# Performance work log

Measured on AMD Instinct MI355X. Metric: run time of the kernel, lower is better.

Reference implementation:

```python
import jax, jax.numpy as jnp
import numpy as np

B, C, H, W = 4, 19, 1024, 1024
N = 500000

def setup_inputs() -> dict:
    key = jax.random.key(0)
    k1, k2, k3, k4, k5 = jax.random.split(key, 5)
    predict = jax.random.normal(k1, (B, C, H, W), dtype=jnp.float32)
    target = jax.random.randint(k2, (B, H, W), 0, C, dtype=jnp.int32)
    loc_b = jax.random.randint(k3, (N,), 0, B, dtype=jnp.int64)
    loc_row = jax.random.randint(k4, (N,), 0, H, dtype=jnp.int64)
    loc_col = jax.random.randint(k5, (N,), 0, W, dtype=jnp.int64)
    return {"predict": predict, "target": target,
            "loc_b": loc_b, "loc_row": loc_row, "loc_col": loc_col}

def reference(predict, target, loc_b, loc_row, loc_col):
    # Faithful to PartialLoss: full softmax over channel dim of the WHOLE
    # tensor, then gather sparse locations, then CrossEntropyLoss (which
    # internally applies log_softmax again to the probabilities).
    pred = jax.nn.softmax(predict, axis=1)            # [B, C, H, W]
    gathered = pred[loc_b, :, loc_row, loc_col]       # [N, C]
    labels = target[loc_b, loc_row, loc_col].astype(jnp.int32)  # [N]
    logp = jax.nn.log_softmax(gathered, axis=-1)      # [N, C]
    nll = -jnp.take_along_axis(logp, labels[:, None], axis=-1)[:, 0]  # [N]
    return jnp.mean(nll)
```

## Files before the change

kernel.cpp:

```cpp
#include <hip/hip_runtime.h>


#define CCH 19
#define BLOCK 256
#define POS_BITS 20
#define TOTAL_POS (4 << POS_BITS)

__device__ __forceinline__ float nll_from_channels(const float* __restrict__ base,
                                                   int label, size_t ch_stride)
{
    float x[CCH];
    #pragma unroll
    for (int j = 0; j < CCH; ++j) x[j] = base[(size_t)j * ch_stride];

    float m = x[0];
    #pragma unroll
    for (int j = 1; j < CCH; ++j) m = fmaxf(m, x[j]);

    float s = 0.0f, e_label = 0.0f;
    #pragma unroll
    for (int j = 0; j < CCH; ++j) {
        float e = __expf(x[j] - m);
        s += e;
        if (j == label) e_label = e;
        x[j] = e;
    }
    float inv = 1.0f / s;

    float s2 = 0.0f;
    #pragma unroll
    for (int j = 0; j < CCH; ++j) s2 += __expf(x[j] * inv);

    return __logf(s2) - e_label * inv;
}

__global__ __launch_bounds__(BLOCK) void nll_table_kernel(
    const float* __restrict__ predict,
    const int* __restrict__ target,
    float* __restrict__ table)
{
    int i = blockIdx.x * blockDim.x + threadIdx.x;
    if (i >= TOTAL_POS) return;
    int b = i >> POS_BITS;
    int pos = i & ((1 << POS_BITS) - 1);
    const float* base = predict + (((size_t)b * CCH) << POS_BITS) + (size_t)pos;
    table[i] = nll_from_channels(base, target[i], (size_t)1 << POS_BITS);
}

__global__ __launch_bounds__(BLOCK) void table_gather_kernel(
    const float* __restrict__ table,
    const int* __restrict__ loc_b,
    const int* __restrict__ loc_row,
    const int* __restrict__ loc_col,
    float* __restrict__ partial,
    int n)
{
    int i = blockIdx.x * blockDim.x + threadIdx.x;
    float nll = 0.0f;
    if (i < n) {
        int idx = (loc_b[i] << POS_BITS) + (loc_row[i] << 10) + loc_col[i];
        nll = table[idx];
    }
    __shared__ float red[BLOCK];
    red[threadIdx.x] = nll;
    __syncthreads();
    #pragma unroll
    for (int off = BLOCK / 2; off > 0; off >>= 1) {
        if (threadIdx.x < off) red[threadIdx.x] += red[threadIdx.x + off];
        __syncthreads();
    }
    if (threadIdx.x == 0) partial[blockIdx.x] = red[0];
}

__global__ __launch_bounds__(BLOCK) void partial_loss_gather(
    const float* __restrict__ predict,
    const int* __restrict__ target,
    const int* __restrict__ loc_b,
    const int* __restrict__ loc_row,
    const int* __restrict__ loc_col,
    float* __restrict__ partial,
    int n)
{
    int i = blockIdx.x * blockDim.x + threadIdx.x;
    float nll = 0.0f;
    if (i < n) {
        int b = loc_b[i];
        int pos = (loc_row[i] << 10) + loc_col[i];
        const float* base = predict + (((size_t)b * CCH) << POS_BITS) + (size_t)pos;
        int label = target[((size_t)b << POS_BITS) + (size_t)pos];
        nll = nll_from_channels(base, label, (size_t)1 << POS_BITS);
    }
    __shared__ float red[BLOCK];
    red[threadIdx.x] = nll;
    __syncthreads();
    #pragma unroll
    for (int off = BLOCK / 2; off > 0; off >>= 1) {
        if (threadIdx.x < off) red[threadIdx.x] += red[threadIdx.x + off];
        __syncthreads();
    }
    if (threadIdx.x == 0) partial[blockIdx.x] = red[0];
}

__global__ __launch_bounds__(BLOCK) void partial_loss_finalize(
    const float* __restrict__ partial,
    int nparts,
    float* __restrict__ out,
    float inv_n)
{
    __shared__ double red[BLOCK];
    double acc = 0.0;
    for (int i = threadIdx.x; i < nparts; i += BLOCK) acc += (double)partial[i];
    red[threadIdx.x] = acc;
    __syncthreads();
    #pragma unroll
    for (int off = BLOCK / 2; off > 0; off >>= 1) {
        if (threadIdx.x < off) red[threadIdx.x] += red[threadIdx.x + off];
        __syncthreads();
    }
    if (threadIdx.x == 0) out[0] = (float)(red[0] * (double)inv_n);
}

extern "C" void kernel_launch(void* const* d_in, const int* in_sizes, int n_in,
                              void* d_out, int out_size, void* d_ws, size_t ws_size,
                              hipStream_t stream)
{
    const float* predict = (const float*)d_in[0];
    const int*   target  = (const int*)d_in[1];
    const int*   loc_b   = (const int*)d_in[2];
    const int*   loc_row = (const int*)d_in[3];
    const int*   loc_col = (const int*)d_in[4];
    float* out = (float*)d_out;

    int n = in_sizes[2];
    int nblocks = (n + BLOCK - 1) / BLOCK;

    size_t table_bytes = (size_t)TOTAL_POS * sizeof(float);
    size_t partial_bytes = (size_t)nblocks * sizeof(float);

    if (ws_size >= table_bytes + partial_bytes) {
        float* table   = (float*)d_ws;
        float* partial = (float*)((char*)d_ws + table_bytes);
        int tblocks = (TOTAL_POS + BLOCK - 1) / BLOCK;
        nll_table_kernel<<<tblocks, BLOCK, 0, stream>>>(predict, target, table);
        table_gather_kernel<<<nblocks, BLOCK, 0, stream>>>(
            table, loc_b, loc_row, loc_col, partial, n);
        partial_loss_finalize<<<1, BLOCK, 0, stream>>>(
            partial, nblocks, out, 1.0f / (float)n);
    } else {
        float* partial = (float*)d_ws;
        partial_loss_gather<<<nblocks, BLOCK, 0, stream>>>(
            predict, target, loc_b, loc_row, loc_col, partial, n);
        partial_loss_finalize<<<1, BLOCK, 0, stream>>>(
            partial, nblocks, out, 1.0f / (float)n);
    }
}
```

Baseline: 87.75 us.

## Compute NLL table only for 16-position chunks touched by sampled locations

Adds a byte mask over 16-position chunks. It is cleared and built from the sampled locations, and the table kernel skips threads whose chunk is unmarked. This is meant to cut predict-tensor reads for positions never gathered. With 500k random samples over about 4M positions, most chunks are still touched, and memory lines may be shared with touched chunks, so the saving in traffic may be small. Two extra kernel launches and a scattered byte-write pass are added in exchange.

```diff
diff --git a/kernel.cpp b/kernel.cpp
--- a/kernel.cpp
+++ b/kernel.cpp
@@ -5,14 +5,10 @@
 #define BLOCK 256
 #define POS_BITS 20
 #define TOTAL_POS (4 << POS_BITS)
+#define NCHUNK (TOTAL_POS >> 4)
 
-__device__ __forceinline__ float nll_from_channels(const float* __restrict__ base,
-                                                   int label, size_t ch_stride)
+__device__ __forceinline__ float nll_compute(float* __restrict__ x, int label)
 {
-    float x[CCH];
-    #pragma unroll
-    for (int j = 0; j < CCH; ++j) x[j] = base[(size_t)j * ch_stride];
-
     float m = x[0];
     #pragma unroll
     for (int j = 1; j < CCH; ++j) m = fmaxf(m, x[j]);
@@ -34,17 +30,43 @@
     return __logf(s2) - e_label * inv;
 }
 
-__global__ __launch_bounds__(BLOCK) void nll_table_kernel(
+__global__ __launch_bounds__(BLOCK) void clear_mask(unsigned int* __restrict__ mask32)
+{
+    int i = blockIdx.x * blockDim.x + threadIdx.x;
+    mask32[i] = 0u;
+}
+
+__global__ __launch_bounds__(BLOCK) void build_mask(
+    const int* __restrict__ loc_b,
+    const int* __restrict__ loc_row,
+    const int* __restrict__ loc_col,
+    unsigned char* __restrict__ mask,
+    int n)
+{
+    int i = blockIdx.x * blockDim.x + threadIdx.x;
+    if (i < n) {
+        int idx = (loc_b[i] << POS_BITS) + (loc_row[i] << 10) + loc_col[i];
+        mask[idx >> 4] = 1;
+    }
+}
+
+__global__ __launch_bounds__(BLOCK) void nll_table_masked(
     const float* __restrict__ predict,
     const int* __restrict__ target,
+    const unsigned char* __restrict__ mask,
     float* __restrict__ table)
 {
     int i = blockIdx.x * blockDim.x + threadIdx.x;
-    if (i >= TOTAL_POS) return;
+    if (!mask[i >> 4]) return;
     int b = i >> POS_BITS;
     int pos = i & ((1 << POS_BITS) - 1);
     const float* base = predict + (((size_t)b * CCH) << POS_BITS) + (size_t)pos;
-    table[i] = nll_from_channels(base, target[i], (size_t)1 << POS_BITS);
+
+    float x[CCH];
+    #pragma unroll
+    for (int j = 0; j < CCH; ++j) x[j] = base[(size_t)j << POS_BITS];
+
+    table[i] = nll_compute(x, target[i]);
 }
 
 __global__ __launch_bounds__(BLOCK) void table_gather_kernel(
@@ -88,7 +110,10 @@
         int pos = (loc_row[i] << 10) + loc_col[i];
         const float* base = predict + (((size_t)b * CCH) << POS_BITS) + (size_t)pos;
         int label = target[((size_t)b << POS_BITS) + (size_t)pos];
-        nll = nll_from_channels(base, label, (size_t)1 << POS_BITS);
+        float x[CCH];
+        #pragma unroll
+        for (int j = 0; j < CCH; ++j) x[j] = base[(size_t)j << POS_BITS];
+        nll = nll_compute(x, label);
     }
     __shared__ float red[BLOCK];
     red[threadIdx.x] = nll;
@@ -134,14 +159,19 @@
     int n = in_sizes[2];
     int nblocks = (n + BLOCK - 1) / BLOCK;
 
-    size_t table_bytes = (size_t)TOTAL_POS * sizeof(float);
-    size_t partial_bytes = (size_t)nblocks * sizeof(float);
+    size_t table_bytes   = (size_t)TOTAL_POS * sizeof(float);
+    size_t partial_bytes = (size_t)((nblocks + 63) & ~63) * sizeof(float);
+    size_t mask_bytes    = (size_t)NCHUNK;
 
-    if (ws_size >= table_bytes + partial_bytes) {
-        float* table   = (float*)d_ws;
-        float* partial = (float*)((char*)d_ws + table_bytes);
-        int tblocks = (TOTAL_POS + BLOCK - 1) / BLOCK;
-        nll_table_kernel<<<tblocks, BLOCK, 0, stream>>>(predict, target, table);
+    if (ws_size >= table_bytes + partial_bytes + mask_bytes) {
+        float*         table   = (float*)d_ws;
+        float*         partial = (float*)((char*)d_ws + table_bytes);
+        unsigned char* mask    = (unsigned char*)d_ws + table_bytes + partial_bytes;
+
+        clear_mask<<<NCHUNK / 4 / BLOCK, BLOCK, 0, stream>>>((unsigned int*)mask);
+        build_mask<<<nblocks, BLOCK, 0, stream>>>(loc_b, loc_row, loc_col, mask, n);
+        nll_table_masked<<<TOTAL_POS / BLOCK, BLOCK, 0, stream>>>(
+            predict, target, mask, table);
         table_gather_kernel<<<nblocks, BLOCK, 0, stream>>>(
             table, loc_b, loc_row, loc_col, partial, n);
         partial_loss_finalize<<<1, BLOCK, 0, stream>>>(
```

New measurement: 95.34 us. 8.6% more time.

## Replace dense NLL table with per-position hit counts and masked reduction

Applied to the files above, without the earlier changes.

Instead of computing NLL for every pixel into a float table and then gathering it, the code builds a byte-packed histogram of how often each position is sampled, using atomics on 32-bit words. It then scans all positions, loads the 19 channels only where the count is nonzero, and accumulates count-weighted NLL directly into block partials. About 11% of positions are hit, so most channel loads are skipped. The trade-offs are an extra clear kernel, atomic contention, and 8-bit counters that would overflow past 255 hits per position.

```diff
diff --git a/kernel.cpp b/kernel.cpp
--- a/kernel.cpp
+++ b/kernel.cpp
@@ -5,14 +5,10 @@
 #define BLOCK 256
 #define POS_BITS 20
 #define TOTAL_POS (4 << POS_BITS)
+#define NBLK_A (TOTAL_POS / BLOCK)
 
-__device__ __forceinline__ float nll_from_channels(const float* __restrict__ base,
-                                                   int label, size_t ch_stride)
+__device__ __forceinline__ float nll_compute(float* __restrict__ x, int label)
 {
-    float x[CCH];
-    #pragma unroll
-    for (int j = 0; j < CCH; ++j) x[j] = base[(size_t)j * ch_stride];
-
     float m = x[0];
     #pragma unroll
     for (int j = 1; j < CCH; ++j) m = fmaxf(m, x[j]);
@@ -34,35 +30,47 @@
     return __logf(s2) - e_label * inv;
 }
 
-__global__ __launch_bounds__(BLOCK) void nll_table_kernel(
-    const float* __restrict__ predict,
-    const int* __restrict__ target,
-    float* __restrict__ table)
+__global__ __launch_bounds__(BLOCK) void clear_counts(unsigned int* __restrict__ cnt32)
 {
     int i = blockIdx.x * blockDim.x + threadIdx.x;
-    if (i >= TOTAL_POS) return;
-    int b = i >> POS_BITS;
-    int pos = i & ((1 << POS_BITS) - 1);
-    const float* base = predict + (((size_t)b * CCH) << POS_BITS) + (size_t)pos;
-    table[i] = nll_from_channels(base, target[i], (size_t)1 << POS_BITS);
+    cnt32[i] = 0u;
 }
 
-__global__ __launch_bounds__(BLOCK) void table_gather_kernel(
-    const float* __restrict__ table,
+__global__ __launch_bounds__(BLOCK) void build_counts(
     const int* __restrict__ loc_b,
     const int* __restrict__ loc_row,
     const int* __restrict__ loc_col,
-    float* __restrict__ partial,
+    unsigned int* __restrict__ cnt32,
     int n)
 {
     int i = blockIdx.x * blockDim.x + threadIdx.x;
-    float nll = 0.0f;
     if (i < n) {
         int idx = (loc_b[i] << POS_BITS) + (loc_row[i] << 10) + loc_col[i];
-        nll = table[idx];
+        atomicAdd(&cnt32[idx >> 2], 1u << ((idx & 3) << 3));
     }
+}
+
+__global__ __launch_bounds__(BLOCK) void nll_count_reduce(
+    const float* __restrict__ predict,
+    const int* __restrict__ target,
+    const unsigned char* __restrict__ counts,
+    float* __restrict__ partial)
+{
+    int i = blockIdx.x * blockDim.x + threadIdx.x;
+    int cnt = counts[i];
+    float contrib = 0.0f;
+    if (cnt) {
+        int b = i >> POS_BITS;
+        int pos = i & ((1 << POS_BITS) - 1);
+        const float* base = predict + (((size_t)b * CCH) << POS_BITS) + (size_t)pos;
+        float x[CCH];
+        #pragma unroll
+        for (int j = 0; j < CCH; ++j) x[j] = base[(size_t)j << POS_BITS];
+        contrib = (float)cnt * nll_compute(x, target[i]);
+    }
+
     __shared__ float red[BLOCK];
-    red[threadIdx.x] = nll;
+    red[threadIdx.x] = contrib;
     __syncthreads();
     #pragma unroll
     for (int off = BLOCK / 2; off > 0; off >>= 1) {
@@ -88,7 +96,10 @@
         int pos = (loc_row[i] << 10) + loc_col[i];
         const float* base = predict + (((size_t)b * CCH) << POS_BITS) + (size_t)pos;
         int label = target[((size_t)b << POS_BITS) + (size_t)pos];
-        nll = nll_from_channels(base, label, (size_t)1 << POS_BITS);
+        float x[CCH];
+        #pragma unroll
+        for (int j = 0; j < CCH; ++j) x[j] = base[(size_t)j << POS_BITS];
+        nll = nll_compute(x, label);
     }
     __shared__ float red[BLOCK];
     red[threadIdx.x] = nll;
@@ -134,18 +145,19 @@
     int n = in_sizes[2];
     int nblocks = (n + BLOCK - 1) / BLOCK;
 
-    size_t table_bytes = (size_t)TOTAL_POS * sizeof(float);
-    size_t partial_bytes = (size_t)nblocks * sizeof(float);
+    size_t count_bytes   = (size_t)TOTAL_POS;
+    size_t partial_bytes = (size_t)NBLK_A * sizeof(float);
 
-    if (ws_size >= table_bytes + partial_bytes) {
-        float* table   = (float*)d_ws;
-        float* partial = (float*)((char*)d_ws + table_bytes);
-        int tblocks = (TOTAL_POS + BLOCK - 1) / BLOCK;
-        nll_table_kernel<<<tblocks, BLOCK, 0, stream>>>(predict, target, table);
-        table_gather_kernel<<<nblocks, BLOCK, 0, stream>>>(
-            table, loc_b, loc_row, loc_col, partial, n);
+    if (ws_size >= count_bytes + partial_bytes) {
+        unsigned int* cnt32   = (unsigned int*)d_ws;
+        float*        partial = (float*)((char*)d_ws + count_bytes);
+
+        clear_counts<<<TOTAL_POS / 4 / BLOCK, BLOCK, 0, stream>>>(cnt32);
+        build_counts<<<nblocks, BLOCK, 0, stream>>>(loc_b, loc_row, loc_col, cnt32, n);
+        nll_count_reduce<<<NBLK_A, BLOCK, 0, stream>>>(
+            predict, target, (const unsigned char*)cnt32, partial);
         partial_loss_finalize<<<1, BLOCK, 0, stream>>>(
-            partial, nblocks, out, 1.0f / (float)n);
+            partial, NBLK_A, out, 1.0f / (float)n);
     } else {
         float* partial = (float*)d_ws;
         partial_loss_gather<<<nblocks, BLOCK, 0, stream>>>(
```

New measurement: 110.9 us. 26.4% more time.
